# Performance work log

Hardware: AMD Instinct MI355X
Metric: run time of the kernel (lower is better)

The kernel has to match this reference:

```python
import jax, jax.numpy as jnp
import numpy as np
from jax import lax

ALPHA = 4.0  # spikingjelly default Sigmoid surrogate alpha
EPS = 1e-5

@jax.custom_vjp
def spike_fn(u):
    return (u >= 0.0).astype(u.dtype)

def _spike_fwd(u):
    return spike_fn(u), u

def _spike_bwd(u, g):
    sg = jax.nn.sigmoid(ALPHA * u)
    return (g * ALPHA * sg * (1.0 - sg),)

spike_fn.defvjp(_spike_fwd, _spike_bwd)

def if_node(x):
    """Multi-step IF neuron (v_threshold=1, hard reset to 0) over leading T dim."""
    def step(v, xt):
        v = v + xt
        s = spike_fn(v - 1.0)
        v = v * (1.0 - s)
        return v, s
    _, spikes = lax.scan(step, jnp.zeros_like(x[0]), x)
    return spikes

def layer_norm(x, g, b):
    m = jnp.mean(x, axis=-1, keepdims=True)
    var = jnp.mean((x - m) ** 2, axis=-1, keepdims=True)
    return (x - m) * lax.rsqrt(var + EPS) * g + b

def setup_inputs() -> dict:
    key = jax.random.key(0)
    T, B, S, D = 4, 8, 1024, 768
    ks = jax.random.split(key, 5)
    scale = 1.0 / np.sqrt(D)
    inp = {
        "x": jax.random.normal(ks[0], (T, B, S, D), jnp.float32),
        "wq": jax.random.normal(ks[1], (D, D), jnp.float32) * scale,
        "wk": jax.random.normal(ks[2], (D, D), jnp.float32) * scale,
        "wv": jax.random.normal(ks[3], (D, D), jnp.float32) * scale,
        "wo": jax.random.normal(ks[4], (D, D), jnp.float32) * scale,
        "gq": jnp.ones((D,), jnp.float32), "bq": jnp.zeros((D,), jnp.float32),
        "gk": jnp.ones((D,), jnp.float32), "bk": jnp.zeros((D,), jnp.float32),
        "gv": jnp.ones((D,), jnp.float32), "bv": jnp.zeros((D,), jnp.float32),
        "go": jnp.ones((D,), jnp.float32), "bo": jnp.zeros((D,), jnp.float32),
    }
    return inp

def reference(x, wq, wk, wv, wo, gq, bq, gk, bk, gv, bv, go, bo):
    T, B, S, D = x.shape
    H, HD = 12, 64
    tmp = if_node(x)                                   # [T,B,S,D] spikes
    Q = if_node(layer_norm(tmp @ wq, gq, bq))
    K = if_node(layer_norm(tmp @ wk, gk, bk))
    V = if_node(layer_norm(tmp @ wv, gv, bv))
    # [T,B,S,H,HD] -> [T,B,H,S,HD]
    Q = Q.reshape(T, B, S, H, HD).transpose(0, 1, 3, 2, 4)
    K = K.reshape(T, B, S, H, HD).transpose(0, 1, 3, 2, 4)
    V = V.reshape(T, B, S, H, HD).transpose(0, 1, 3, 2, 4)
    QK = jnp.sum(Q * K, axis=-2, keepdims=True)        # [T,B,H,1,HD]
    QK = if_node(QK)                                   # talking_heads IF spikes
    QKV = V * QK                                       # broadcast over S
    QKV = QKV.transpose(0, 1, 3, 2, 4).reshape(T, B, S, D)
    return layer_norm(QKV @ wo, go, bo)
```

## Files before the change

kernel.cpp:

```cpp
#include <hip/hip_runtime.h>
#include <hip/hip_bf16.h>

#define T_ 4
#define B_ 8
#define S_ 1024
#define D_ 768
#define BS_ (B_*S_)
#define M_ (T_*B_*S_)
#define BSD_ (B_*S_*D_)
#define LN_EPS 1e-5f
#define TAU 4e-5f

typedef unsigned short u16;
typedef unsigned char u8;
typedef unsigned int u32;
typedef unsigned long long u64;
typedef __bf16 bf16x8 __attribute__((ext_vector_type(8)));
typedef float f32x4 __attribute__((ext_vector_type(4)));

__global__ __launch_bounds__(768)
void k_if_mask(const float* __restrict__ x, u64* __restrict__ Am, u16* __restrict__ Ab) {
    int bs = blockIdx.x;
    int d = threadIdx.x;
    int wv = d >> 6, lane = d & 63;
    float v = 0.f;
    for (int t = 0; t < T_; ++t) {
        v += x[(size_t)t * BSD_ + (size_t)bs * D_ + d];
        bool s = (v >= 1.0f);
        u64 m = __ballot(s);
        if (lane == 0) Am[((size_t)t * 12 + wv) * BS_ + bs] = m;
        Ab[(size_t)t * BSD_ + (size_t)bs * D_ + d] = s ? 0x3F80 : 0;
        if (s) v = 0.f;
    }
}

__global__ void k_wconv(const float* __restrict__ wq, const float* __restrict__ wk,
                        const float* __restrict__ wv, const float* __restrict__ wo,
                        u16* __restrict__ Whi, u16* __restrict__ Wlo, u16* __restrict__ Wo) {
    int idx = blockIdx.x * 256 + threadIdx.x;
    int mat = idx / (D_ * D_);
    int r = idx % (D_ * D_);
    int n = r / D_;
    int k = r % D_;
    const float* src = (mat == 0) ? wq : (mat == 1) ? wk : (mat == 2) ? wv : wo;
    float w = src[k * D_ + n];
    __bf16 hi = (__bf16)w;
    u16 uhi = __builtin_bit_cast(u16, hi);
    if (mat == 3) { Wo[r] = uhi; return; }
    float lo = w - (float)hi;
    u16 ulo = __builtin_bit_cast(u16, (__bf16)lo);
    Whi[(size_t)mat * D_ * D_ + r] = uhi;
    Wlo[(size_t)mat * D_ * D_ + r] = ulo;
}

__device__ __forceinline__ void gload16(const void* g, void* l) {
    __builtin_amdgcn_global_load_lds(
        (const __attribute__((address_space(1))) unsigned int*)g,
        (__attribute__((address_space(3))) unsigned int*)l, 16, 0, 0);
}

template<int NMATS>
__global__ __launch_bounds__(256)
void k_gemm(const u16* __restrict__ A, const u16* __restrict__ Bhi,
            const u16* __restrict__ Blo, float* __restrict__ C, int ntn, int N) {
    __shared__ __align__(16) u16 As[128 * 64];
    __shared__ __align__(16) u16 Bh[128 * 64];
    __shared__ __align__(16) u16 Bl[NMATS == 2 ? 128 * 64 : 8];
    int bid = blockIdx.x;
    bid = (bid & 7) * (gridDim.x >> 3) + (bid >> 3);
    int bn = bid % ntn, bm = bid / ntn;
    int tid = threadIdx.x;
    int l = tid & 63, w = tid >> 6;
    int wr = w >> 1, wc = w & 1;
    int lan16 = l & 15, kh = l >> 4;

    f32x4 acc[4][4];
    #pragma unroll
    for (int m = 0; m < 4; ++m)
        #pragma unroll
        for (int n = 0; n < 4; ++n)
            #pragma unroll
            for (int r = 0; r < 4; ++r) acc[m][n][r] = 0.f;

    int srow[4], scol[4];
    #pragma unroll
    for (int j = 0; j < 4; ++j) {
        int li = j * 256 + tid;
        srow[j] = li >> 3;
        scol[j] = ((li & 7) ^ ((li >> 3) & 7)) * 8;
    }
    int wbase = (tid >> 6) << 10;

    int aoff[4][2], boff[4][2];
    #pragma unroll
    for (int m = 0; m < 4; ++m)
        #pragma unroll
        for (int s = 0; s < 2; ++s) {
            int Ra = wr * 64 + m * 16 + lan16;
            aoff[m][s] = Ra * 128 + (((s * 4 + kh) ^ (Ra & 7)) << 4);
            int Rb = wc * 64 + m * 16 + lan16;
            boff[m][s] = Rb * 128 + (((s * 4 + kh) ^ (Rb & 7)) << 4);
        }

    for (int kk = 0; kk < 768; kk += 64) {
        #pragma unroll
        for (int j = 0; j < 4; ++j) {
            gload16(A   + (size_t)(bm * 128 + srow[j]) * 768 + kk + scol[j],
                    (char*)As + j * 4096 + wbase);
            gload16(Bhi + (size_t)(bn * 128 + srow[j]) * 768 + kk + scol[j],
                    (char*)Bh + j * 4096 + wbase);
            if (NMATS == 2)
                gload16(Blo + (size_t)(bn * 128 + srow[j]) * 768 + kk + scol[j],
                        (char*)Bl + j * 4096 + wbase);
        }
        __syncthreads();
        #pragma unroll
        for (int s = 0; s < 2; ++s) {
            bf16x8 af[4], bh[4], bl[4];
            #pragma unroll
            for (int m = 0; m < 4; ++m)
                af[m] = *(const bf16x8*)((const char*)As + aoff[m][s]);
            #pragma unroll
            for (int n = 0; n < 4; ++n) {
                bh[n] = *(const bf16x8*)((const char*)Bh + boff[n][s]);
                if (NMATS == 2) bl[n] = *(const bf16x8*)((const char*)Bl + boff[n][s]);
            }
            #pragma unroll
            for (int m = 0; m < 4; ++m)
                #pragma unroll
                for (int n = 0; n < 4; ++n) {
                    acc[m][n] = __builtin_amdgcn_mfma_f32_16x16x32_bf16(af[m], bh[n], acc[m][n], 0, 0, 0);
                    if (NMATS == 2)
                        acc[m][n] = __builtin_amdgcn_mfma_f32_16x16x32_bf16(af[m], bl[n], acc[m][n], 0, 0, 0);
                }
        }
        __syncthreads();
    }
    #pragma unroll
    for (int m = 0; m < 4; ++m)
        #pragma unroll
        for (int n = 0; n < 4; ++n)
            #pragma unroll
            for (int r = 0; r < 4; ++r) {
                int crow = bm * 128 + wr * 64 + m * 16 + kh * 4 + r;
                int ccol = bn * 128 + wc * 64 + n * 16 + lan16;
                C[(size_t)crow * N + ccol] = acc[m][n][r];
            }
}

__global__ __launch_bounds__(256)
void k_lnif(const float* __restrict__ Y, const float* __restrict__ g,
            const float* __restrict__ bt, u8* __restrict__ Sp,
            int* __restrict__ rowlist, int* __restrict__ cnt, int mat) {
    #pragma clang fp contract(off)
    int row = blockIdx.x * 4 + (threadIdx.x >> 6);
    int lane = threadIdx.x & 63;
    float v[12];
    #pragma unroll
    for (int i = 0; i < 12; ++i) v[i] = 0.f;
    float gv[12], bv[12];
    #pragma unroll
    for (int i = 0; i < 12; ++i) { gv[i] = g[lane + 64*i]; bv[i] = bt[lane + 64*i]; }
    bool fl = false;
    for (int t = 0; t < T_; ++t) {
        size_t base = ((size_t)t * BS_ + row) * D_;
        float xv[12];
        double s = 0.0;
        #pragma unroll
        for (int i = 0; i < 12; ++i) { xv[i] = Y[base + lane + 64*i]; s += (double)xv[i]; }
        #pragma unroll
        for (int o = 1; o < 64; o <<= 1) s += __shfl_xor(s, o, 64);
        s = __shfl(s, 0, 64);
        float m = (float)(s / 768.0);
        float d[12];
        double q = 0.0;
        #pragma unroll
        for (int i = 0; i < 12; ++i) { d[i] = xv[i] - m; float sq = d[i]*d[i]; q += (double)sq; }
        #pragma unroll
        for (int o = 1; o < 64; o <<= 1) q += __shfl_xor(q, o, 64);
        q = __shfl(q, 0, 64);
        float var = (float)(q / 768.0);
        float inv = 1.0f / __fsqrt_rn(var + LN_EPS);
        #pragma unroll
        for (int i = 0; i < 12; ++i) {
            float yn = ((d[i] * inv) * gv[i]) + bv[i];
            v[i] += yn;
            fl = fl || (fabsf(v[i] - 1.0f) < TAU);
            bool sp = (v[i] >= 1.0f);
            Sp[base + lane + 64*i] = sp ? (u8)1 : (u8)0;
            if (sp) v[i] = 0.f;
        }
    }
    u64 bal = __ballot(fl);
    if (lane == 0 && bal != 0ull) {
        int slot = atomicAdd(cnt + mat, 1);
        rowlist[mat * BS_ + slot] = row;
    }
}

__global__ __launch_bounds__(768)
void k_repairT(const u64* __restrict__ Am,
               const float* __restrict__ wq, const float* __restrict__ wk,
               const float* __restrict__ wv,
               const float* __restrict__ gq, const float* __restrict__ bq,
               const float* __restrict__ gk, const float* __restrict__ bk,
               const float* __restrict__ gv, const float* __restrict__ bv,
               u8* __restrict__ Qs, u8* __restrict__ Ks, u8* __restrict__ Vs,
               const int* __restrict__ rowlist, const int* __restrict__ cnt) {
    #pragma clang fp contract(off)
    int mat = blockIdx.y;
    if (blockIdx.x >= cnt[mat]) return;
    int row = rowlist[mat * BS_ + blockIdx.x];
    const float* W = (mat == 0) ? wq : (mat == 1) ? wk : wv;
    const float* g = (mat == 0) ? gq : (mat == 1) ? gk : gv;
    const float* bb = (mat == 0) ? bq : (mat == 1) ? bk : bv;
    u8* Sp = (mat == 0) ? Qs : (mat == 1) ? Ks : Vs;
    const float4* Wv4 = (const float4*)W;

    __shared__ u64 mks[4][12];
    __shared__ int pops[4][12];
    __shared__ int cnt4[4];
    __shared__ u16 idxs[4][768];
    __shared__ float4 ys[4][192];
    __shared__ float2 mi_sh[4];
    __shared__ double redd[12];

    int tid = threadIdx.x;
    int t = tid / 192;
    int tg = tid % 192;

    if (tid < 48) {
        int tt = tid / 12, kw = tid % 12;
        u64 m = Am[((size_t)tt * 12 + kw) * BS_ + row];
        mks[tt][kw] = m;
        pops[tt][kw] = __popcll(m);
    }
    __syncthreads();
    if (tid < 48) {
        int tt = tid / 12, kw = tid % 12;
        int off = 0;
        for (int j = 0; j < kw; ++j) off += pops[tt][j];
        u64 m = mks[tt][kw];
        int kb0 = kw * 64;
        while (m) {
            int kb = __builtin_ctzll(m);
            m &= m - 1;
            idxs[tt][off++] = (u16)(kb0 + kb);
        }
        if (kw == 11) cnt4[tt] = off;
    }
    __syncthreads();

    int cn = cnt4[t];
    float y0 = 0.f, y1 = 0.f, y2 = 0.f, y3 = 0.f;
    const u16* il = idxs[t];
    #pragma unroll 8
    for (int i = 0; i < cn; ++i) {
        float4 w = Wv4[(size_t)il[i] * 192 + tg];
        y0 += w.x; y1 += w.y; y2 += w.z; y3 += w.w;
    }

    int lane = tid & 63;
    int wv_t = tg >> 6;
    double s = (double)y0 + (double)y1 + (double)y2 + (double)y3;
    #pragma unroll
    for (int o = 1; o < 64; o <<= 1) s += __shfl_xor(s, o, 64);
    if (lane == 0) redd[t * 3 + wv_t] = s;
    __syncthreads();
    double stot = redd[t * 3] + redd[t * 3 + 1] + redd[t * 3 + 2];
    float mean = (float)(stot / 768.0);
    float d0 = y0 - mean, d1 = y1 - mean, d2 = y2 - mean, d3 = y3 - mean;
    double q = (double)(d0*d0) + (double)(d1*d1) + (double)(d2*d2) + (double)(d3*d3);
    #pragma unroll
    for (int o = 1; o < 64; o <<= 1) q += __shfl_xor(q, o, 64);
    __syncthreads();
    if (lane == 0) redd[t * 3 + wv_t] = q;
    __syncthreads();
    double qtot = redd[t * 3] + redd[t * 3 + 1] + redd[t * 3 + 2];
    float var = (float)(qtot / 768.0);
    float inv = 1.0f / __fsqrt_rn(var + LN_EPS);

    ys[t][tg] = make_float4(y0, y1, y2, y3);
    if (tg == 0) mi_sh[t] = make_float2(mean, inv);
    __syncthreads();

    if (tid < 192) {
        float4 gd = ((const float4*)g)[tg];
        float4 bd = ((const float4*)bb)[tg];
        float4 yt[4];
        float2 mi[4];
        #pragma unroll
        for (int tt = 0; tt < 4; ++tt) { yt[tt] = ys[tt][tg]; mi[tt] = mi_sh[tt]; }
        uchar4 o4[4];
        #pragma unroll
        for (int j = 0; j < 4; ++j) {
            float gj = (j == 0) ? gd.x : (j == 1) ? gd.y : (j == 2) ? gd.z : gd.w;
            float bj = (j == 0) ? bd.x : (j == 1) ? bd.y : (j == 2) ? bd.z : bd.w;
            float v = 0.f;
            #pragma unroll
            for (int tt = 0; tt < 4; ++tt) {
                float yj = (j == 0) ? yt[tt].x : (j == 1) ? yt[tt].y : (j == 2) ? yt[tt].z : yt[tt].w;
                float d = yj - mi[tt].x;
                float yn = ((d * mi[tt].y) * gj) + bj;
                v += yn;
                bool sp = (v >= 1.0f);
                u8 sb = sp ? (u8)1 : (u8)0;
                if (j == 0) o4[tt].x = sb;
                if (j == 1) o4[tt].y = sb;
                if (j == 2) o4[tt].z = sb;
                if (j == 3) o4[tt].w = sb;
                if (sp) v = 0.f;
            }
        }
        #pragma unroll
        for (int tt = 0; tt < 4; ++tt)
            *(uchar4*)(Sp + ((size_t)tt * BS_ + row) * D_ + tg * 4) = o4[tt];
    }
}

__global__ void k_qkred(const u8* __restrict__ Q, const u8* __restrict__ K,
                        float* __restrict__ QK) {
    int bid = blockIdx.x;
    int sg = bid & 31, tb = bid >> 5;
    int tid = threadIdx.x;
    int c4 = tid * 4;
    size_t base = (size_t)tb * S_ * D_ + (size_t)sg * 32 * D_;
    int acc[4] = {0, 0, 0, 0};
    for (int s = 0; s < 32; ++s) {
        uchar4 q = *(const uchar4*)(Q + base + (size_t)s * D_ + c4);
        uchar4 k = *(const uchar4*)(K + base + (size_t)s * D_ + c4);
        acc[0] += q.x & k.x; acc[1] += q.y & k.y; acc[2] += q.z & k.z; acc[3] += q.w & k.w;
    }
    float* dst = QK + (size_t)tb * D_ + c4;
    #pragma unroll
    for (int j = 0; j < 4; ++j) atomicAdd(dst + j, (float)acc[j]);
}

__global__ void k_qkif(const float* __restrict__ QK, u8* __restrict__ QKs) {
    int i = blockIdx.x * 256 + threadIdx.x;
    float v = 0.f;
    for (int t = 0; t < T_; ++t) {
        v += QK[t * (B_ * D_) + i];
        bool s = (v >= 1.0f);
        QKs[t * (B_ * D_) + i] = s ? 1 : 0;
        if (s) v = 0.f;
    }
}

__global__ void k_qkv(const u8* __restrict__ V, const u8* __restrict__ QKs,
                      u16* __restrict__ O) {
    size_t e = ((size_t)blockIdx.x * 256 + threadIdx.x) * 4;
    uchar4 v = *(const uchar4*)(V + e);
    size_t d = e % D_;
    size_t b = (e / ((size_t)S_ * D_)) % B_;
    size_t t = e / BSD_;
    uchar4 qk = *(const uchar4*)(QKs + t * (B_ * D_) + b * D_ + d);
    ushort4 o;
    o.x = (v.x & qk.x) ? 0x3F80 : 0;
    o.y = (v.y & qk.y) ? 0x3F80 : 0;
    o.z = (v.z & qk.z) ? 0x3F80 : 0;
    o.w = (v.w & qk.w) ? 0x3F80 : 0;
    *(ushort4*)(O + e) = o;
}

__device__ __forceinline__ float block_sum(float v, float* red) {
    #pragma unroll
    for (int o = 32; o > 0; o >>= 1) v += __shfl_down(v, o, 64);
    int lane = threadIdx.x & 63, w = threadIdx.x >> 6;
    __syncthreads();
    if (lane == 0) red[w] = v;
    __syncthreads();
    return (red[0] + red[1]) + (red[2] + red[3]);
}

__global__ __launch_bounds__(256)
void k_lnfinal(const float* __restrict__ Y, const float* __restrict__ g,
               const float* __restrict__ bt, float* __restrict__ out) {
    #pragma clang fp contract(off)
    __shared__ float red[4];
    size_t row = (size_t)blockIdx.x * D_;
    int tid = threadIdx.x;
    float y[3];
    float s = 0.f;
    #pragma unroll
    for (int j = 0; j < 3; ++j) { y[j] = Y[row + tid + j * 256]; s += y[j]; }
    float mean = block_sum(s, red) / 768.0f;
    float q = 0.f;
    #pragma unroll
    for (int j = 0; j < 3; ++j) { float d = y[j] - mean; q += d * d; }
    float var = block_sum(q, red) / 768.0f;
    float inv = 1.0f / __fsqrt_rn(var + LN_EPS);
    #pragma unroll
    for (int j = 0; j < 3; ++j) {
        int c = tid + j * 256;
        out[row + c] = (y[j] - mean) * inv * g[c] + bt[c];
    }
}

extern "C" void kernel_launch(void* const* d_in, const int* in_sizes, int n_in,
                              void* d_out, int out_size, void* d_ws, size_t ws_size,
                              hipStream_t stream) {
    const float* x  = (const float*)d_in[0];
    const float* wq = (const float*)d_in[1];
    const float* wk = (const float*)d_in[2];
    const float* wv = (const float*)d_in[3];
    const float* wo = (const float*)d_in[4];
    const float* gq = (const float*)d_in[5];
    const float* bq = (const float*)d_in[6];
    const float* gk = (const float*)d_in[7];
    const float* bk = (const float*)d_in[8];
    const float* gv = (const float*)d_in[9];
    const float* bv = (const float*)d_in[10];
    const float* go = (const float*)d_in[11];
    const float* bo = (const float*)d_in[12];
    float* out = (float*)d_out;

    char* ws = (char*)d_ws;
    size_t off = 0;
    auto alloc = [&](size_t bytes) -> void* {
        void* p = ws + off;
        off += (bytes + 255) & ~(size_t)255;
        return p;
    };
    u64* Am    = (u64*)alloc((size_t)T_ * 12 * BS_ * 8);
    u16* Ab    = (u16*)alloc((size_t)M_ * D_ * 2);
    float* Y   = (float*)alloc((size_t)M_ * D_ * 4);
    u8* Qs     = (u8*)alloc((size_t)M_ * D_);
    u8* Ks     = (u8*)alloc((size_t)M_ * D_);
    u8* Vs     = (u8*)alloc((size_t)M_ * D_);
    u16* Whi   = (u16*)alloc((size_t)3 * D_ * D_ * 2);
    u16* Wlo   = (u16*)alloc((size_t)3 * D_ * D_ * 2);
    u16* Wo    = (u16*)alloc((size_t)D_ * D_ * 2);
    float* QK  = (float*)alloc((size_t)T_ * B_ * D_ * 4);
    u8* QKs    = (u8*)alloc((size_t)T_ * B_ * D_);
    int* rowlist = (int*)alloc((size_t)3 * BS_ * 4);
    int* cnt   = (int*)alloc(256);

    hipMemsetAsync(QK, 0, (size_t)T_ * B_ * D_ * 4, stream);
    hipMemsetAsync(cnt, 0, 12, stream);

    k_if_mask<<<BS_, 768, 0, stream>>>(x, Am, Ab);
    k_wconv<<<(4 * D_ * D_) / 256, 256, 0, stream>>>(wq, wk, wv, wo, Whi, Wlo, Wo);
    const int ntn = D_ / 128;
    const int gemm_grid = (M_ / 128) * ntn;
    k_gemm<2><<<gemm_grid, 256, 0, stream>>>(Ab, Whi + 0 * D_ * D_, Wlo + 0 * D_ * D_, Y, ntn, D_);
    k_lnif<<<BS_ / 4, 256, 0, stream>>>(Y, gq, bq, Qs, rowlist, cnt, 0);
    k_gemm<2><<<gemm_grid, 256, 0, stream>>>(Ab, Whi + 1 * D_ * D_, Wlo + 1 * D_ * D_, Y, ntn, D_);
    k_lnif<<<BS_ / 4, 256, 0, stream>>>(Y, gk, bk, Ks, rowlist, cnt, 1);
    k_gemm<2><<<gemm_grid, 256, 0, stream>>>(Ab, Whi + 2 * D_ * D_, Wlo + 2 * D_ * D_, Y, ntn, D_);
    k_lnif<<<BS_ / 4, 256, 0, stream>>>(Y, gv, bv, Vs, rowlist, cnt, 2);
    k_repairT<<<dim3(BS_, 3), 768, 0, stream>>>(Am, wq, wk, wv, gq, bq, gk, bk, gv, bv,
                                                Qs, Ks, Vs, rowlist, cnt);
    k_qkred<<<T_ * B_ * 32, 192, 0, stream>>>(Qs, Ks, QK);
    k_qkif<<<(B_ * D_) / 256, 256, 0, stream>>>(QK, QKs);
    k_qkv<<<(M_ * D_) / 4 / 256, 256, 0, stream>>>(Vs, QKs, Ab);
    k_gemm<1><<<gemm_grid, 256, 0, stream>>>(Ab, Wo, Wo, Y, ntn, D_);
    k_lnfinal<<<M_, 256, 0, stream>>>(Y, go, bo, out);
}
```

Baseline: 552.2 us.

## Replace GEMM with 256x256-tile double-buffered kernel and batch Q/K projections

The 128x128 GEMM is replaced by a 512-thread kernel computing 256x256 tiles. It double-buffers 64-wide K slices in LDS through direct global-to-LDS loads, waits with explicit vmcnt, and raises wave priority around the MFMA blocks. The hi/lo split-bf16 weights are handled as a 24-step K loop rather than two MFMAs per step. When workspace allows, Q and K projections launch together in one 2D grid with a second output buffer. The goal is more operand reuse per tile, load/compute overlap, and fewer tail effects, at the cost of 128KB LDS per block and higher register pressure.

```diff
diff --git a/kernel.cpp b/kernel.cpp
--- a/kernel.cpp
+++ b/kernel.cpp
@@ -59,92 +59,119 @@
         (__attribute__((address_space(3))) unsigned int*)l, 16, 0, 0);
 }
 
-template<int NMATS>
-__global__ __launch_bounds__(256)
-void k_gemm(const u16* __restrict__ A, const u16* __restrict__ Bhi,
-            const u16* __restrict__ Blo, float* __restrict__ C, int ntn, int N) {
-    __shared__ __align__(16) u16 As[128 * 64];
-    __shared__ __align__(16) u16 Bh[128 * 64];
-    __shared__ __align__(16) u16 Bl[NMATS == 2 ? 128 * 64 : 8];
+template<int NT>
+__global__ __launch_bounds__(512, 2)
+void k_gemm8(const u16* __restrict__ A,
+             const u16* __restrict__ Bhi0, const u16* __restrict__ Blo0,
+             const u16* __restrict__ Bhi1, const u16* __restrict__ Blo1,
+             float* __restrict__ C0, float* __restrict__ C1) {
+    __shared__ __align__(16) char ldsb[131072];
+    const u16* Bhi = blockIdx.y ? Bhi1 : Bhi0;
+    const u16* Blo = blockIdx.y ? Blo1 : Blo0;
+    float* C = blockIdx.y ? C1 : C0;
     int bid = blockIdx.x;
-    bid = (bid & 7) * (gridDim.x >> 3) + (bid >> 3);
-    int bn = bid % ntn, bm = bid / ntn;
+    bid = (bid & 7) * 48 + (bid >> 3);
+    int bn = bid % 3, bm = bid / 3;
     int tid = threadIdx.x;
-    int l = tid & 63, w = tid >> 6;
-    int wr = w >> 1, wc = w & 1;
-    int lan16 = l & 15, kh = l >> 4;
-
-    f32x4 acc[4][4];
-    #pragma unroll
-    for (int m = 0; m < 4; ++m)
+    int wid = tid >> 6, l = tid & 63;
+    int wm = wid >> 2, wn = wid & 3;
+    int lan16 = l & 15, q = l >> 4;
+
+    f32x4 acc[8][4];
+    #pragma unroll
+    for (int m = 0; m < 8; ++m)
         #pragma unroll
         for (int n = 0; n < 4; ++n)
             #pragma unroll
             for (int r = 0; r < 4; ++r) acc[m][n][r] = 0.f;
 
-    int srow[4], scol[4];
-    #pragma unroll
-    for (int j = 0; j < 4; ++j) {
-        int li = j * 256 + tid;
-        srow[j] = li >> 3;
-        scol[j] = ((li & 7) ^ ((li >> 3) & 7)) * 8;
-    }
-    int wbase = (tid >> 6) << 10;
-
-    int aoff[4][2], boff[4][2];
-    #pragma unroll
-    for (int m = 0; m < 4; ++m)
-        #pragma unroll
-        for (int s = 0; s < 2; ++s) {
-            int Ra = wr * 64 + m * 16 + lan16;
-            aoff[m][s] = Ra * 128 + (((s * 4 + kh) ^ (Ra & 7)) << 4);
-            int Rb = wc * 64 + m * 16 + lan16;
-            boff[m][s] = Rb * 128 + (((s * 4 + kh) ^ (Rb & 7)) << 4);
-        }
-
-    for (int kk = 0; kk < 768; kk += 64) {
-        #pragma unroll
-        for (int j = 0; j < 4; ++j) {
-            gload16(A   + (size_t)(bm * 128 + srow[j]) * 768 + kk + scol[j],
-                    (char*)As + j * 4096 + wbase);
-            gload16(Bhi + (size_t)(bn * 128 + srow[j]) * 768 + kk + scol[j],
-                    (char*)Bh + j * 4096 + wbase);
-            if (NMATS == 2)
-                gload16(Blo + (size_t)(bn * 128 + srow[j]) * 768 + kk + scol[j],
-                        (char*)Bl + j * 4096 + wbase);
-        }
-        __syncthreads();
-        #pragma unroll
-        for (int s = 0; s < 2; ++s) {
-            bf16x8 af[4], bh[4], bl[4];
+    int ch0 = tid, ch1 = tid + 512;
+    int srow0 = ch0 >> 3, scol0 = ((ch0 & 7) ^ ((ch0 >> 3) & 7)) * 8;
+    int srow1 = ch1 >> 3, scol1 = ((ch1 & 7) ^ ((ch1 >> 3) & 7)) * 8;
+
+    int aoff[8][2], boff[4][2];
+    #pragma unroll
+    for (int m = 0; m < 8; ++m)
+        #pragma unroll
+        for (int kb = 0; kb < 2; ++kb) {
+            int r = m * 16 + lan16;
+            aoff[m][kb] = wm * 16384 + r * 128 + (((kb * 4 + q) ^ (r & 7)) << 4);
+        }
+    #pragma unroll
+    for (int n = 0; n < 4; ++n)
+        #pragma unroll
+        for (int kb = 0; kb < 2; ++kb) {
+            int r = (wn & 1) * 64 + n * 16 + lan16;
+            boff[n][kb] = 65536 + (wn >> 1) * 16384 + r * 128 + (((kb * 4 + q) ^ (r & 7)) << 4);
+        }
+
+    auto STAGE = [&](int buf, int kt) {
+        bool hi = (NT == 12) || (kt < 12);
+        int kk = (hi ? kt : kt - 12) * 64;
+        const u16* Bt = hi ? Bhi : Blo;
+        char* lb = ldsb + buf * 32768;
+        #pragma unroll
+        for (int h = 0; h < 2; ++h) {
+            gload16(A  + (size_t)(bm * 256 + h * 128 + srow0) * 768 + kk + scol0, lb + h * 16384 + ch0 * 16);
+            gload16(A  + (size_t)(bm * 256 + h * 128 + srow1) * 768 + kk + scol1, lb + h * 16384 + ch1 * 16);
+            gload16(Bt + (size_t)(bn * 256 + h * 128 + srow0) * 768 + kk + scol0, lb + 65536 + h * 16384 + ch0 * 16);
+            gload16(Bt + (size_t)(bn * 256 + h * 128 + srow1) * 768 + kk + scol1, lb + 65536 + h * 16384 + ch1 * 16);
+        }
+    };
+
+    STAGE(0, 0);
+    STAGE(1, 1);
+    asm volatile("s_waitcnt vmcnt(8)" ::: "memory");
+    __builtin_amdgcn_sched_barrier(0);
+    __builtin_amdgcn_s_barrier();
+
+    int cur = 0;
+    for (int t = 0; t < NT; ++t) {
+        const char* lb = ldsb + cur * 32768;
+        #pragma unroll
+        for (int kb = 0; kb < 2; ++kb) {
+            bf16x8 bfr[4];
             #pragma unroll
-            for (int m = 0; m < 4; ++m)
-                af[m] = *(const bf16x8*)((const char*)As + aoff[m][s]);
+            for (int n = 0; n < 4; ++n)
+                bfr[n] = *(const bf16x8*)(lb + boff[n][kb]);
             #pragma unroll
-            for (int n = 0; n < 4; ++n) {
-                bh[n] = *(const bf16x8*)((const char*)Bh + boff[n][s]);
-                if (NMATS == 2) bl[n] = *(const bf16x8*)((const char*)Bl + boff[n][s]);
+            for (int mg = 0; mg < 2; ++mg) {
+                bf16x8 afr[4];
+                #pragma unroll
+                for (int mm = 0; mm < 4; ++mm)
+                    afr[mm] = *(const bf16x8*)(lb + aoff[mg * 4 + mm][kb]);
+                __builtin_amdgcn_s_setprio(1);
+                #pragma unroll
+                for (int mm = 0; mm < 4; ++mm)
+                    #pragma unroll
+                    for (int n = 0; n < 4; ++n)
+                        acc[mg * 4 + mm][n] = __builtin_amdgcn_mfma_f32_16x16x32_bf16(
+                            afr[mm], bfr[n], acc[mg * 4 + mm][n], 0, 0, 0);
+                __builtin_amdgcn_s_setprio(0);
             }
-            #pragma unroll
-            for (int m = 0; m < 4; ++m)
-                #pragma unroll
-                for (int n = 0; n < 4; ++n) {
-                    acc[m][n] = __builtin_amdgcn_mfma_f32_16x16x32_bf16(af[m], bh[n], acc[m][n], 0, 0, 0);
-                    if (NMATS == 2)
-                        acc[m][n] = __builtin_amdgcn_mfma_f32_16x16x32_bf16(af[m], bl[n], acc[m][n], 0, 0, 0);
-                }
-        }
-        __syncthreads();
-    }
-    #pragma unroll
-    for (int m = 0; m < 4; ++m)
+        }
+        __builtin_amdgcn_sched_barrier(0);
+        __builtin_amdgcn_s_barrier();
+        if (t + 2 < NT) {
+            STAGE(cur, t + 2);
+            asm volatile("s_waitcnt vmcnt(8)" ::: "memory");
+        } else {
+            asm volatile("s_waitcnt vmcnt(0)" ::: "memory");
+        }
+        __builtin_amdgcn_sched_barrier(0);
+        __builtin_amdgcn_s_barrier();
+        cur ^= 1;
+    }
+
+    #pragma unroll
+    for (int m = 0; m < 8; ++m)
         #pragma unroll
         for (int n = 0; n < 4; ++n)
             #pragma unroll
             for (int r = 0; r < 4; ++r) {
-                int crow = bm * 128 + wr * 64 + m * 16 + kh * 4 + r;
-                int ccol = bn * 128 + wc * 64 + n * 16 + lan16;
-                C[(size_t)crow * N + ccol] = acc[m][n][r];
+                int crow = bm * 256 + wm * 128 + m * 16 + q * 4 + r;
+                int ccol = bn * 256 + wn * 64 + n * 16 + lan16;
+                C[(size_t)crow * D_ + ccol] = acc[m][n][r];
             }
 }
 
@@ -435,25 +462,36 @@
     u8* QKs    = (u8*)alloc((size_t)T_ * B_ * D_);
     int* rowlist = (int*)alloc((size_t)3 * BS_ * 4);
     int* cnt   = (int*)alloc(256);
+    size_t base_end = off;
+    float* Y2  = (float*)alloc((size_t)M_ * D_ * 4);
+    bool pair = (off <= ws_size);
+    (void)base_end;
 
     hipMemsetAsync(QK, 0, (size_t)T_ * B_ * D_ * 4, stream);
     hipMemsetAsync(cnt, 0, 12, stream);
 
     k_if_mask<<<BS_, 768, 0, stream>>>(x, Am, Ab);
     k_wconv<<<(4 * D_ * D_) / 256, 256, 0, stream>>>(wq, wk, wv, wo, Whi, Wlo, Wo);
-    const int ntn = D_ / 128;
-    const int gemm_grid = (M_ / 128) * ntn;
-    k_gemm<2><<<gemm_grid, 256, 0, stream>>>(Ab, Whi + 0 * D_ * D_, Wlo + 0 * D_ * D_, Y, ntn, D_);
-    k_lnif<<<BS_ / 4, 256, 0, stream>>>(Y, gq, bq, Qs, rowlist, cnt, 0);
-    k_gemm<2><<<gemm_grid, 256, 0, stream>>>(Ab, Whi + 1 * D_ * D_, Wlo + 1 * D_ * D_, Y, ntn, D_);
-    k_lnif<<<BS_ / 4, 256, 0, stream>>>(Y, gk, bk, Ks, rowlist, cnt, 1);
-    k_gemm<2><<<gemm_grid, 256, 0, stream>>>(Ab, Whi + 2 * D_ * D_, Wlo + 2 * D_ * D_, Y, ntn, D_);
+    const u16* WhiQ = Whi + 0 * D_ * D_; const u16* WloQ = Wlo + 0 * D_ * D_;
+    const u16* WhiK = Whi + 1 * D_ * D_; const u16* WloK = Wlo + 1 * D_ * D_;
+    const u16* WhiV = Whi + 2 * D_ * D_; const u16* WloV = Wlo + 2 * D_ * D_;
+    if (pair) {
+        k_gemm8<24><<<dim3(384, 2), 512, 0, stream>>>(Ab, WhiQ, WloQ, WhiK, WloK, Y, Y2);
+        k_lnif<<<BS_ / 4, 256, 0, stream>>>(Y,  gq, bq, Qs, rowlist, cnt, 0);
+        k_lnif<<<BS_ / 4, 256, 0, stream>>>(Y2, gk, bk, Ks, rowlist, cnt, 1);
+    } else {
+        k_gemm8<24><<<dim3(384, 1), 512, 0, stream>>>(Ab, WhiQ, WloQ, WhiQ, WloQ, Y, Y);
+        k_lnif<<<BS_ / 4, 256, 0, stream>>>(Y, gq, bq, Qs, rowlist, cnt, 0);
+        k_gemm8<24><<<dim3(384, 1), 512, 0, stream>>>(Ab, WhiK, WloK, WhiK, WloK, Y, Y);
+        k_lnif<<<BS_ / 4, 256, 0, stream>>>(Y, gk, bk, Ks, rowlist, cnt, 1);
+    }
+    k_gemm8<24><<<dim3(384, 1), 512, 0, stream>>>(Ab, WhiV, WloV, WhiV, WloV, Y, Y);
     k_lnif<<<BS_ / 4, 256, 0, stream>>>(Y, gv, bv, Vs, rowlist, cnt, 2);
     k_repairT<<<dim3(BS_, 3), 768, 0, stream>>>(Am, wq, wk, wv, gq, bq, gk, bk, gv, bv,
                                                 Qs, Ks, Vs, rowlist, cnt);
     k_qkred<<<T_ * B_ * 32, 192, 0, stream>>>(Qs, Ks, QK);
     k_qkif<<<(B_ * D_) / 256, 256, 0, stream>>>(QK, QKs);
     k_qkv<<<(M_ * D_) / 4 / 256, 256, 0, stream>>>(Vs, QKs, Ab);
-    k_gemm<1><<<gemm_grid, 256, 0, stream>>>(Ab, Wo, Wo, Y, ntn, D_);
+    k_gemm8<12><<<dim3(384, 1), 512, 0, stream>>>(Ab, Wo, Wo, Wo, Wo, Y, Y);
     k_lnfinal<<<M_, 256, 0, stream>>>(Y, go, bo, out);
 }
```

After: 622.8 us. 12.8% more time.

## Batch Q/K/V GEMMs and LN-IF into single launches; grid-stride repair kernel

Applied to the files above, without the earlier changes.

Runs the three Q/K/V projection GEMMs as one launch with a blockIdx.y selector and separate output buffers, and does the same for the three LayerNorm+IF passes, when the workspace is large enough. This removes launch gaps and tail effects between the serial kernels and gives each launch more blocks. The repair kernel now uses a fixed grid of 1024 blocks that stride over the flagged rows instead of launching one block per possible row, most of which exited at once. The cost is two extra full fp32 intermediate buffers, which adds memory footprint and may reduce L2 reuse of the shared A operand.

```diff
diff --git a/kernel.cpp b/kernel.cpp
--- a/kernel.cpp
+++ b/kernel.cpp
@@ -61,11 +61,18 @@
 
 template<int NMATS>
 __global__ __launch_bounds__(256)
-void k_gemm(const u16* __restrict__ A, const u16* __restrict__ Bhi,
-            const u16* __restrict__ Blo, float* __restrict__ C, int ntn, int N) {
+void k_gemm(const u16* __restrict__ A,
+            const u16* __restrict__ Bh0, const u16* __restrict__ Bl0, float* __restrict__ C0,
+            const u16* __restrict__ Bh1, const u16* __restrict__ Bl1, float* __restrict__ C1,
+            const u16* __restrict__ Bh2, const u16* __restrict__ Bl2, float* __restrict__ C2,
+            int ntn, int N) {
     __shared__ __align__(16) u16 As[128 * 64];
     __shared__ __align__(16) u16 Bh[128 * 64];
     __shared__ __align__(16) u16 Bl[NMATS == 2 ? 128 * 64 : 8];
+    int my = blockIdx.y;
+    const u16* Bhi = (my == 0) ? Bh0 : (my == 1) ? Bh1 : Bh2;
+    const u16* Blo = (my == 0) ? Bl0 : (my == 1) ? Bl1 : Bl2;
+    float* C = (my == 0) ? C0 : (my == 1) ? C1 : C2;
     int bid = blockIdx.x;
     bid = (bid & 7) * (gridDim.x >> 3) + (bid >> 3);
     int bn = bid % ntn, bm = bid / ntn;
@@ -149,18 +156,27 @@
 }
 
 __global__ __launch_bounds__(256)
-void k_lnif(const float* __restrict__ Y, const float* __restrict__ g,
-            const float* __restrict__ bt, u8* __restrict__ Sp,
-            int* __restrict__ rowlist, int* __restrict__ cnt, int mat) {
+void k_lnif(const float* __restrict__ Y0, const float* __restrict__ Y1,
+            const float* __restrict__ Y2,
+            const float* __restrict__ gq, const float* __restrict__ bq,
+            const float* __restrict__ gk, const float* __restrict__ bk,
+            const float* __restrict__ gv, const float* __restrict__ bv,
+            u8* __restrict__ Qs, u8* __restrict__ Ks, u8* __restrict__ Vs,
+            int* __restrict__ rowlist, int* __restrict__ cnt, int mat0) {
     #pragma clang fp contract(off)
+    int mat = mat0 + blockIdx.y;
+    const float* Y = (mat == 0) ? Y0 : (mat == 1) ? Y1 : Y2;
+    const float* g = (mat == 0) ? gq : (mat == 1) ? gk : gv;
+    const float* bt = (mat == 0) ? bq : (mat == 1) ? bk : bv;
+    u8* Sp = (mat == 0) ? Qs : (mat == 1) ? Ks : Vs;
     int row = blockIdx.x * 4 + (threadIdx.x >> 6);
     int lane = threadIdx.x & 63;
     float v[12];
     #pragma unroll
     for (int i = 0; i < 12; ++i) v[i] = 0.f;
-    float gv[12], bv[12];
-    #pragma unroll
-    for (int i = 0; i < 12; ++i) { gv[i] = g[lane + 64*i]; bv[i] = bt[lane + 64*i]; }
+    float gv_[12], bv_[12];
+    #pragma unroll
+    for (int i = 0; i < 12; ++i) { gv_[i] = g[lane + 64*i]; bv_[i] = bt[lane + 64*i]; }
     bool fl = false;
     for (int t = 0; t < T_; ++t) {
         size_t base = ((size_t)t * BS_ + row) * D_;
@@ -183,7 +199,7 @@
         float inv = 1.0f / __fsqrt_rn(var + LN_EPS);
         #pragma unroll
         for (int i = 0; i < 12; ++i) {
-            float yn = ((d[i] * inv) * gv[i]) + bv[i];
+            float yn = ((d[i] * inv) * gv_[i]) + bv_[i];
             v[i] += yn;
             fl = fl || (fabsf(v[i] - 1.0f) < TAU);
             bool sp = (v[i] >= 1.0f);
@@ -209,8 +225,7 @@
                const int* __restrict__ rowlist, const int* __restrict__ cnt) {
     #pragma clang fp contract(off)
     int mat = blockIdx.y;
-    if (blockIdx.x >= cnt[mat]) return;
-    int row = rowlist[mat * BS_ + blockIdx.x];
+    int nf = cnt[mat];
     const float* W = (mat == 0) ? wq : (mat == 1) ? wk : wv;
     const float* g = (mat == 0) ? gq : (mat == 1) ? gk : gv;
     const float* bb = (mat == 0) ? bq : (mat == 1) ? bk : bv;
@@ -229,92 +244,97 @@
     int t = tid / 192;
     int tg = tid % 192;
 
-    if (tid < 48) {
-        int tt = tid / 12, kw = tid % 12;
-        u64 m = Am[((size_t)tt * 12 + kw) * BS_ + row];
-        mks[tt][kw] = m;
-        pops[tt][kw] = __popcll(m);
-    }
-    __syncthreads();
-    if (tid < 48) {
-        int tt = tid / 12, kw = tid % 12;
-        int off = 0;
-        for (int j = 0; j < kw; ++j) off += pops[tt][j];
-        u64 m = mks[tt][kw];
-        int kb0 = kw * 64;
-        while (m) {
-            int kb = __builtin_ctzll(m);
-            m &= m - 1;
-            idxs[tt][off++] = (u16)(kb0 + kb);
-        }
-        if (kw == 11) cnt4[tt] = off;
-    }
-    __syncthreads();
-
-    int cn = cnt4[t];
-    float y0 = 0.f, y1 = 0.f, y2 = 0.f, y3 = 0.f;
-    const u16* il = idxs[t];
-    #pragma unroll 8
-    for (int i = 0; i < cn; ++i) {
-        float4 w = Wv4[(size_t)il[i] * 192 + tg];
-        y0 += w.x; y1 += w.y; y2 += w.z; y3 += w.w;
-    }
-
-    int lane = tid & 63;
-    int wv_t = tg >> 6;
-    double s = (double)y0 + (double)y1 + (double)y2 + (double)y3;
-    #pragma unroll
-    for (int o = 1; o < 64; o <<= 1) s += __shfl_xor(s, o, 64);
-    if (lane == 0) redd[t * 3 + wv_t] = s;
-    __syncthreads();
-    double stot = redd[t * 3] + redd[t * 3 + 1] + redd[t * 3 + 2];
-    float mean = (float)(stot / 768.0);
-    float d0 = y0 - mean, d1 = y1 - mean, d2 = y2 - mean, d3 = y3 - mean;
-    double q = (double)(d0*d0) + (double)(d1*d1) + (double)(d2*d2) + (double)(d3*d3);
-    #pragma unroll
-    for (int o = 1; o < 64; o <<= 1) q += __shfl_xor(q, o, 64);
-    __syncthreads();
-    if (lane == 0) redd[t * 3 + wv_t] = q;
-    __syncthreads();
-    double qtot = redd[t * 3] + redd[t * 3 + 1] + redd[t * 3 + 2];
-    float var = (float)(qtot / 768.0);
-    float inv = 1.0f / __fsqrt_rn(var + LN_EPS);
-
-    ys[t][tg] = make_float4(y0, y1, y2, y3);
-    if (tg == 0) mi_sh[t] = make_float2(mean, inv);
-    __syncthreads();
-
-    if (tid < 192) {
-        float4 gd = ((const float4*)g)[tg];
-        float4 bd = ((const float4*)bb)[tg];
-        float4 yt[4];
-        float2 mi[4];
-        #pragma unroll
-        for (int tt = 0; tt < 4; ++tt) { yt[tt] = ys[tt][tg]; mi[tt] = mi_sh[tt]; }
-        uchar4 o4[4];
-        #pragma unroll
-        for (int j = 0; j < 4; ++j) {
-            float gj = (j == 0) ? gd.x : (j == 1) ? gd.y : (j == 2) ? gd.z : gd.w;
-            float bj = (j == 0) ? bd.x : (j == 1) ? bd.y : (j == 2) ? bd.z : bd.w;
-            float v = 0.f;
-            #pragma unroll
-            for (int tt = 0; tt < 4; ++tt) {
-                float yj = (j == 0) ? yt[tt].x : (j == 1) ? yt[tt].y : (j == 2) ? yt[tt].z : yt[tt].w;
-                float d = yj - mi[tt].x;
-                float yn = ((d * mi[tt].y) * gj) + bj;
-                v += yn;
-                bool sp = (v >= 1.0f);
-                u8 sb = sp ? (u8)1 : (u8)0;
-                if (j == 0) o4[tt].x = sb;
-                if (j == 1) o4[tt].y = sb;
-                if (j == 2) o4[tt].z = sb;
-                if (j == 3) o4[tt].w = sb;
-                if (sp) v = 0.f;
+    for (int e = blockIdx.x; e < nf; e += gridDim.x) {
+        int row = rowlist[mat * BS_ + e];
+
+        if (tid < 48) {
+            int tt = tid / 12, kw = tid % 12;
+            u64 m = Am[((size_t)tt * 12 + kw) * BS_ + row];
+            mks[tt][kw] = m;
+            pops[tt][kw] = __popcll(m);
+        }
+        __syncthreads();
+        if (tid < 48) {
+            int tt = tid / 12, kw = tid % 12;
+            int off = 0;
+            for (int j = 0; j < kw; ++j) off += pops[tt][j];
+            u64 m = mks[tt][kw];
+            int kb0 = kw * 64;
+            while (m) {
+                int kb = __builtin_ctzll(m);
+                m &= m - 1;
+                idxs[tt][off++] = (u16)(kb0 + kb);
             }
-        }
-        #pragma unroll
-        for (int tt = 0; tt < 4; ++tt)
-            *(uchar4*)(Sp + ((size_t)tt * BS_ + row) * D_ + tg * 4) = o4[tt];
+            if (kw == 11) cnt4[tt] = off;
+        }
+        __syncthreads();
+
+        int cn = cnt4[t];
+        float y0 = 0.f, y1 = 0.f, y2 = 0.f, y3 = 0.f;
+        const u16* il = idxs[t];
+        #pragma unroll 8
+        for (int i = 0; i < cn; ++i) {
+            float4 w = Wv4[(size_t)il[i] * 192 + tg];
+            y0 += w.x; y1 += w.y; y2 += w.z; y3 += w.w;
+        }
+
+        int lane = tid & 63;
+        int wv_t = tg >> 6;
+        double s = (double)y0 + (double)y1 + (double)y2 + (double)y3;
+        #pragma unroll
+        for (int o = 1; o < 64; o <<= 1) s += __shfl_xor(s, o, 64);
+        if (lane == 0) redd[t * 3 + wv_t] = s;
+        __syncthreads();
+        double stot = redd[t * 3] + redd[t * 3 + 1] + redd[t * 3 + 2];
+        float mean = (float)(stot / 768.0);
+        float d0 = y0 - mean, d1 = y1 - mean, d2 = y2 - mean, d3 = y3 - mean;
+        double q = (double)(d0*d0) + (double)(d1*d1) + (double)(d2*d2) + (double)(d3*d3);
+        #pragma unroll
+        for (int o = 1; o < 64; o <<= 1) q += __shfl_xor(q, o, 64);
+        __syncthreads();
+        if (lane == 0) redd[t * 3 + wv_t] = q;
+        __syncthreads();
+        double qtot = redd[t * 3] + redd[t * 3 + 1] + redd[t * 3 + 2];
+        float var = (float)(qtot / 768.0);
+        float inv = 1.0f / __fsqrt_rn(var + LN_EPS);
+
+        ys[t][tg] = make_float4(y0, y1, y2, y3);
+        if (tg == 0) mi_sh[t] = make_float2(mean, inv);
+        __syncthreads();
+
+        if (tid < 192) {
+            float4 gd = ((const float4*)g)[tg];
+            float4 bd = ((const float4*)bb)[tg];
+            float4 yt[4];
+            float2 mi[4];
+            #pragma unroll
+            for (int tt = 0; tt < 4; ++tt) { yt[tt] = ys[tt][tg]; mi[tt] = mi_sh[tt]; }
+            uchar4 o4[4];
+            #pragma unroll
+            for (int j = 0; j < 4; ++j) {
+                float gj = (j == 0) ? gd.x : (j == 1) ? gd.y : (j == 2) ? gd.z : gd.w;
+                float bj = (j == 0) ? bd.x : (j == 1) ? bd.y : (j == 2) ? bd.z : bd.w;
+                float v = 0.f;
+                #pragma unroll
+                for (int tt = 0; tt < 4; ++tt) {
+                    float yj = (j == 0) ? yt[tt].x : (j == 1) ? yt[tt].y : (j == 2) ? yt[tt].z : yt[tt].w;
+                    float d = yj - mi[tt].x;
+                    float yn = ((d * mi[tt].y) * gj) + bj;
+                    v += yn;
+                    bool sp = (v >= 1.0f);
+                    u8 sb = sp ? (u8)1 : (u8)0;
+                    if (j == 0) o4[tt].x = sb;
+                    if (j == 1) o4[tt].y = sb;
+                    if (j == 2) o4[tt].z = sb;
+                    if (j == 3) o4[tt].w = sb;
+                    if (sp) v = 0.f;
+                }
+            }
+            #pragma unroll
+            for (int tt = 0; tt < 4; ++tt)
+                *(uchar4*)(Sp + ((size_t)tt * BS_ + row) * D_ + tg * 4) = o4[tt];
+        }
+        __syncthreads();
     }
 }
 
@@ -424,7 +444,7 @@
     };
     u64* Am    = (u64*)alloc((size_t)T_ * 12 * BS_ * 8);
     u16* Ab    = (u16*)alloc((size_t)M_ * D_ * 2);
-    float* Y   = (float*)alloc((size_t)M_ * D_ * 4);
+    float* Y0  = (float*)alloc((size_t)M_ * D_ * 4);
     u8* Qs     = (u8*)alloc((size_t)M_ * D_);
     u8* Ks     = (u8*)alloc((size_t)M_ * D_);
     u8* Vs     = (u8*)alloc((size_t)M_ * D_);
@@ -435,6 +455,10 @@
     u8* QKs    = (u8*)alloc((size_t)T_ * B_ * D_);
     int* rowlist = (int*)alloc((size_t)3 * BS_ * 4);
     int* cnt   = (int*)alloc(256);
+    float* Y1  = (float*)alloc((size_t)M_ * D_ * 4);
+    float* Y2  = (float*)alloc((size_t)M_ * D_ * 4);
+    bool fused = (off <= ws_size);
+    if (!fused) { Y1 = Y0; Y2 = Y0; }
 
     hipMemsetAsync(QK, 0, (size_t)T_ * B_ * D_ * 4, stream);
     hipMemsetAsync(cnt, 0, 12, stream);
@@ -443,17 +467,34 @@
     k_wconv<<<(4 * D_ * D_) / 256, 256, 0, stream>>>(wq, wk, wv, wo, Whi, Wlo, Wo);
     const int ntn = D_ / 128;
     const int gemm_grid = (M_ / 128) * ntn;
-    k_gemm<2><<<gemm_grid, 256, 0, stream>>>(Ab, Whi + 0 * D_ * D_, Wlo + 0 * D_ * D_, Y, ntn, D_);
-    k_lnif<<<BS_ / 4, 256, 0, stream>>>(Y, gq, bq, Qs, rowlist, cnt, 0);
-    k_gemm<2><<<gemm_grid, 256, 0, stream>>>(Ab, Whi + 1 * D_ * D_, Wlo + 1 * D_ * D_, Y, ntn, D_);
-    k_lnif<<<BS_ / 4, 256, 0, stream>>>(Y, gk, bk, Ks, rowlist, cnt, 1);
-    k_gemm<2><<<gemm_grid, 256, 0, stream>>>(Ab, Whi + 2 * D_ * D_, Wlo + 2 * D_ * D_, Y, ntn, D_);
-    k_lnif<<<BS_ / 4, 256, 0, stream>>>(Y, gv, bv, Vs, rowlist, cnt, 2);
-    k_repairT<<<dim3(BS_, 3), 768, 0, stream>>>(Am, wq, wk, wv, gq, bq, gk, bk, gv, bv,
-                                                Qs, Ks, Vs, rowlist, cnt);
+    const u16* WhiQ = Whi + 0 * D_ * D_; const u16* WloQ = Wlo + 0 * D_ * D_;
+    const u16* WhiK = Whi + 1 * D_ * D_; const u16* WloK = Wlo + 1 * D_ * D_;
+    const u16* WhiV = Whi + 2 * D_ * D_; const u16* WloV = Wlo + 2 * D_ * D_;
+    if (fused) {
+        k_gemm<2><<<dim3(gemm_grid, 3), 256, 0, stream>>>(Ab,
+            WhiQ, WloQ, Y0, WhiK, WloK, Y1, WhiV, WloV, Y2, ntn, D_);
+        k_lnif<<<dim3(BS_ / 4, 3), 256, 0, stream>>>(Y0, Y1, Y2,
+            gq, bq, gk, bk, gv, bv, Qs, Ks, Vs, rowlist, cnt, 0);
+    } else {
+        k_gemm<2><<<dim3(gemm_grid, 1), 256, 0, stream>>>(Ab,
+            WhiQ, WloQ, Y0, WhiQ, WloQ, Y0, WhiQ, WloQ, Y0, ntn, D_);
+        k_lnif<<<dim3(BS_ / 4, 1), 256, 0, stream>>>(Y0, Y0, Y0,
+            gq, bq, gk, bk, gv, bv, Qs, Ks, Vs, rowlist, cnt, 0);
+        k_gemm<2><<<dim3(gemm_grid, 1), 256, 0, stream>>>(Ab,
+            WhiK, WloK, Y0, WhiK, WloK, Y0, WhiK, WloK, Y0, ntn, D_);
+        k_lnif<<<dim3(BS_ / 4, 1), 256, 0, stream>>>(Y0, Y0, Y0,
+            gq, bq, gk, bk, gv, bv, Qs, Ks, Vs, rowlist, cnt, 1);
+        k_gemm<2><<<dim3(gemm_grid, 1), 256, 0, stream>>>(Ab,
+            WhiV, WloV, Y0, WhiV, WloV, Y0, WhiV, WloV, Y0, ntn, D_);
+        k_lnif<<<dim3(BS_ / 4, 1), 256, 0, stream>>>(Y0, Y0, Y0,
+            gq, bq, gk, bk, gv, bv, Qs, Ks, Vs, rowlist, cnt, 2);
+    }
+    k_repairT<<<dim3(1024, 3), 768, 0, stream>>>(Am, wq, wk, wv, gq, bq, gk, bk, gv, bv,
+                                                 Qs, Ks, Vs, rowlist, cnt);
     k_qkred<<<T_ * B_ * 32, 192, 0, stream>>>(Qs, Ks, QK);
     k_qkif<<<(B_ * D_) / 256, 256, 0, stream>>>(QK, QKs);
     k_qkv<<<(M_ * D_) / 4 / 256, 256, 0, stream>>>(Vs, QKs, Ab);
-    k_gemm<1><<<gemm_grid, 256, 0, stream>>>(Ab, Wo, Wo, Y, ntn, D_);
-    k_lnfinal<<<M_, 256, 0, stream>>>(Y, go, bo, out);
-}
+    k_gemm<1><<<dim3(gemm_grid, 1), 256, 0, stream>>>(Ab,
+        Wo, Wo, Y0, Wo, Wo, Y0, Wo, Wo, Y0, ntn, D_);
+    k_lnfinal<<<M_, 256, 0, stream>>>(Y0, go, bo, out);
+}
```

After: 572.9 us. 1.04x slower.
